# Kernel optimization log

Hardware: AMD Instinct MI355X
Metric: run time of the kernel (lower is better)

## Reference

```python
import jax, jax.numpy as jnp
import numpy as np

# ---- hash-grid constants (from tcnn Encoding config in __init__) ----
N_LEVELS = 16
F = 2                      # n_features_per_level
LOG2_T = 19
T = 1 << LOG2_T            # hashmap entries per level
BASE_RES = 16
PER_LEVEL_SCALE = 1.447269237440378
PRIMES = np.array([1, 2654435761, 805459861], dtype=np.uint32)
# corner offsets of the unit cube, shape [8, 3]
OFFS = np.stack(np.meshgrid([0, 1], [0, 1], [0, 1], indexing='ij'), -1).reshape(8, 3)


def hash_grid_encode(x01, table):
    """x01: [N,3] in [0,1]; table: [L, T, F]. Returns [N, L*F]."""
    offs = jnp.asarray(OFFS, dtype=jnp.int32)          # [8,3]
    primes = jnp.asarray(PRIMES)                       # [3] uint32
    feats = []
    for l in range(N_LEVELS):
        scale = BASE_RES * (PER_LEVEL_SCALE ** l) - 1.0   # tcnn grid scale
        res = int(np.ceil(scale)) + 1                      # grid resolution
        pos = x01 * scale + 0.5                            # [N,3]
        pos0 = jnp.floor(pos)
        w = pos - pos0                                     # trilinear fracs [N,3]
        pos0 = pos0.astype(jnp.int32)
        corners = jnp.clip(pos0[:, None, :] + offs[None], 0, res - 1)  # [N,8,3]
        if res ** 3 <= T:
            # dense (stride) indexing fits in the table
            idx = (corners[..., 0]
                   + res * corners[..., 1]
                   + res * res * corners[..., 2]).astype(jnp.int32)    # [N,8]
        else:
            # spatial hash with uint32 wraparound multiply + xor
            cu = corners.astype(jnp.uint32)
            idx = ((cu[..., 0] * primes[0])
                   ^ (cu[..., 1] * primes[1])
                   ^ (cu[..., 2] * primes[2])) & jnp.uint32(T - 1)
            idx = idx.astype(jnp.int32)
        # trilinear weights: prod over dims of (w if offset==1 else 1-w)
        wc = jnp.where(offs[None].astype(bool), w[:, None, :], 1.0 - w[:, None, :])
        wc = wc.prod(-1)                                   # [N,8]
        g = table[l][idx]                                  # gather -> [N,8,F]
        feats.append(jnp.einsum('nc,ncf->nf', wc, g))      # [N,F]
    return jnp.concatenate(feats, -1)                      # [N, L*F]


def mlp2(x, w1, w2):
    # 2-layer bias-free MLP with ReLU, matching MLP(num_layers=2, bias=False)
    return jnp.maximum(x @ w1, 0.0) @ w2


def setup_inputs() -> dict:
    key = jax.random.key(0)
    ks = jax.random.split(key, 6)
    N = 1048576
    points = jax.random.uniform(ks[0], (N, 3), jnp.float32, -1.0, 1.0)  # in bbox [-1,1]^3
    # tcnn hash-grid init: uniform(-1e-4, 1e-4)
    hash_table = jax.random.uniform(ks[1], (N_LEVELS, T, F), jnp.float32, -1e-4, 1e-4)
    enc_dim = N_LEVELS * F  # 32
    dw1 = jax.random.normal(ks[2], (enc_dim, 64), jnp.float32) * (1.0 / np.sqrt(enc_dim))
    dw2 = jax.random.normal(ks[3], (64, 1), jnp.float32) * (1.0 / 8.0)
    fw1 = jax.random.normal(ks[4], (enc_dim, 64), jnp.float32) * (1.0 / np.sqrt(enc_dim))
    fw2 = jax.random.normal(ks[5], (64, 3), jnp.float32) * (1.0 / 8.0)
    return {"points": points, "hash_table": hash_table,
            "dw1": dw1, "dw2": dw2, "fw1": fw1, "fw2": fw2}


def reference(points, hash_table, dw1, dw2, fw1, fw2):
    # contract_to_unisphere with bbox [[-1,-1,-1],[1,1,1]] -> [0,1]^3, clamped
    x01 = jnp.clip((points + 1.0) * 0.5, 0.0, 1.0)
    enc = hash_grid_encode(x01, hash_table)               # [N, 32]
    density = jax.nn.softplus(mlp2(enc, dw1, dw2))        # [N, 1]
    color = jax.nn.sigmoid(mlp2(enc, fw1, fw2))           # [N, 3]
    return color, density
```

## Files before the change

### kernel.cpp

```cpp
#include <hip/hip_runtime.h>
#include <hip/hip_bf16.h>
#include <cmath>

#define NLV 16
#define TBL_SIZE (1u << 19)

#define SORT_PPB 8192
#define SORT_THREADS 512
#define SORT_NKEYS 4096

#define KB15 32768
#define PPB2 4096
#define GS_THREADS 1024

struct LevelConsts {
    float scale[NLV];
    int   res[NLV];
    int   dense[NLV];
};

__device__ __forceinline__ unsigned int f32_to_bf16_rne(float f) {
    unsigned int u = __float_as_uint(f);
    return (u + 0x7FFFu + ((u >> 16) & 1u)) >> 16;
}
__device__ __forceinline__ unsigned int pack_bf16(float a, float b) {
    return f32_to_bf16_rne(a) | (f32_to_bf16_rne(b) << 16);
}
__device__ __forceinline__ short f32_to_bf16_s(float f) {
    return (short)f32_to_bf16_rne(f);
}
__device__ __forceinline__ float bf16lo_to_f32(unsigned int g) {
    return __uint_as_float(g << 16);
}
__device__ __forceinline__ float bf16hi_to_f32(unsigned int g) {
    return __uint_as_float(g & 0xFFFF0000u);
}

typedef __attribute__((ext_vector_type(8))) short bf16x8;
typedef __attribute__((ext_vector_type(4))) float f32x4;
typedef __attribute__((ext_vector_type(2))) unsigned int u32x2;
typedef __attribute__((ext_vector_type(4))) unsigned int u32x4;

__device__ __forceinline__ unsigned spread3(unsigned x) {
    x &= 0x3FFu;
    x = (x | (x << 16)) & 0x030000FFu;
    x = (x | (x << 8))  & 0x0300F00Fu;
    x = (x | (x << 4))  & 0x030C30C3u;
    x = (x | (x << 2))  & 0x09249249u;
    return x;
}
__device__ __forceinline__ unsigned key12(float px, float py, float pz) {
    float x = fminf(fmaxf((px + 1.0f) * 0.5f, 0.0f), 1.0f);
    float y = fminf(fmaxf((py + 1.0f) * 0.5f, 0.0f), 1.0f);
    float z = fminf(fmaxf((pz + 1.0f) * 0.5f, 0.0f), 1.0f);
    int ix = min((int)(x * 16.0f), 15);
    int iy = min((int)(y * 16.0f), 15);
    int iz = min((int)(z * 16.0f), 15);
    return spread3((unsigned)ix) | (spread3((unsigned)iy) << 1) | (spread3((unsigned)iz) << 2);
}
__device__ __forceinline__ unsigned key15(float px, float py, float pz) {
    float x = fminf(fmaxf((px + 1.0f) * 0.5f, 0.0f), 1.0f);
    float y = fminf(fmaxf((py + 1.0f) * 0.5f, 0.0f), 1.0f);
    float z = fminf(fmaxf((pz + 1.0f) * 0.5f, 0.0f), 1.0f);
    int ix = min((int)(x * 32.0f), 31);
    int iy = min((int)(y * 32.0f), 31);
    int iz = min((int)(z * 32.0f), 31);
    return spread3((unsigned)ix) | (spread3((unsigned)iy) << 1) | (spread3((unsigned)iz) << 2);
}

__global__ __launch_bounds__(GS_THREADS) void cvt_and_hist(
    const float* __restrict__ tablef32, unsigned int* __restrict__ tbl_out, int npairs,
    const float* __restrict__ pts, unsigned int* __restrict__ colpre32,
    int N, int histBlocks)
{
    __shared__ unsigned packed[KB15 / 2];
    if ((int)blockIdx.x < histBlocks) {
        const int blk = blockIdx.x, base = blk * PPB2, cnt = min(PPB2, N - base);
        const int tid = threadIdx.x;
        for (int i = tid; i < KB15 / 2; i += GS_THREADS) packed[i] = 0u;
        __syncthreads();
#pragma unroll
        for (int q = 0; q < PPB2 / GS_THREADS; q++) {
            int idx = q * GS_THREADS + tid;
            if (idx < cnt) {
                int p = base + idx;
                unsigned k = key15(pts[3 * p + 0], pts[3 * p + 1], pts[3 * p + 2]);
                atomicAdd(&packed[k >> 1], (k & 1u) ? 0x10000u : 1u);
            }
        }
        __syncthreads();
        for (int i = tid; i < KB15 / 2; i += GS_THREADS)
            colpre32[(size_t)blk * (KB15 / 2) + i] = packed[i];
    } else {
        int b = blockIdx.x - histBlocks;
        int n2 = npairs >> 1;
        int i = b * GS_THREADS + threadIdx.x;
        int stride = ((int)gridDim.x - histBlocks) * GS_THREADS;
        const f32x4* in4 = (const f32x4*)tablef32;
        u32x2* out2 = (u32x2*)tbl_out;
        for (; i < n2; i += stride) {
            f32x4 v = __builtin_nontemporal_load(&in4[i]);
            u32x2 o;
            o.x = pack_bf16(v.x, v.y);
            o.y = pack_bf16(v.z, v.w);
            __builtin_nontemporal_store(o, &out2[i]);
        }
    }
}

__global__ __launch_bounds__(GS_THREADS) void colscan(
    unsigned int* __restrict__ colpre32, unsigned int* __restrict__ tot, int nblk)
{
    int k2 = blockIdx.x * GS_THREADS + threadIdx.x;
    unsigned run0 = 0, run1 = 0;
    for (int b = 0; b < nblk; b++) {
        size_t off = (size_t)b * (KB15 / 2) + k2;
        unsigned v = colpre32[off];
        colpre32[off] = run0 | (run1 << 16);
        run0 += v & 0xFFFFu;
        run1 += v >> 16;
    }
    tot[2 * k2 + 0] = run0;
    tot[2 * k2 + 1] = run1;
}

__global__ __launch_bounds__(GS_THREADS) void scan_tot(unsigned int* __restrict__ tot) {
    __shared__ unsigned wsum[GS_THREADS / 64];
    const int t = threadIdx.x, lane = t & 63, wid = t >> 6;
    unsigned loc[KB15 / GS_THREADS];
    unsigned s = 0;
#pragma unroll
    for (int j = 0; j < KB15 / GS_THREADS; j++) { loc[j] = tot[t * (KB15 / GS_THREADS) + j]; s += loc[j]; }
    unsigned x = s;
#pragma unroll
    for (int d = 1; d < 64; d <<= 1) {
        unsigned y = __shfl_up(x, d, 64);
        if (lane >= d) x += y;
    }
    unsigned wex = x - s;
    if (lane == 63) wsum[wid] = x;
    __syncthreads();
    if (t == 0) {
        unsigned r = 0;
        for (int i = 0; i < GS_THREADS / 64; i++) { unsigned tt = wsum[i]; wsum[i] = r; r += tt; }
    }
    __syncthreads();
    unsigned run = wex + wsum[wid];
#pragma unroll
    for (int j = 0; j < KB15 / GS_THREADS; j++) { tot[t * (KB15 / GS_THREADS) + j] = run; run += loc[j]; }
}

__global__ __launch_bounds__(GS_THREADS) void global_scatter(
    const float* __restrict__ pts, const unsigned int* __restrict__ colpre32,
    const unsigned int* __restrict__ tot, f32x4* __restrict__ spts4, int N)
{
    __shared__ unsigned packed[KB15 / 2];
    const int blk = blockIdx.x, base = blk * PPB2, cnt = min(PPB2, N - base);
    const int tid = threadIdx.x;
    for (int i = tid; i < KB15 / 2; i += GS_THREADS) packed[i] = 0u;
    __syncthreads();
#pragma unroll
    for (int q = 0; q < PPB2 / GS_THREADS; q++) {
        int idx = q * GS_THREADS + tid;
        if (idx < cnt) {
            int p = base + idx;
            float px = pts[3 * p + 0];
            float py = pts[3 * p + 1];
            float pz = pts[3 * p + 2];
            unsigned k = key15(px, py, pz);
            unsigned old = atomicAdd(&packed[k >> 1], (k & 1u) ? 0x10000u : 1u);
            unsigned rank = (old >> ((k & 1u) * 16)) & 0xFFFFu;
            unsigned cb = colpre32[(size_t)blk * (KB15 / 2) + (k >> 1)];
            unsigned colbase = (k & 1u) ? (cb >> 16) : (cb & 0xFFFFu);
            unsigned pos = tot[k] + colbase + rank;
            f32x4 o;
            o.x = px; o.y = py; o.z = pz; o.w = __uint_as_float((unsigned)p);
            spts4[pos] = o;
        }
    }
}

__global__ __launch_bounds__(SORT_THREADS) void cvt_and_sort(
    const float* __restrict__ tablef32, unsigned int* __restrict__ tbl_out, int npairs,
    const float* __restrict__ pts, f32x4* __restrict__ spts4, int N, int sortBlocks)
{
    __shared__ unsigned hist[SORT_NKEYS];
    __shared__ unsigned wsum[SORT_THREADS / 64];

    if ((int)blockIdx.x < sortBlocks) {
        const int sb   = blockIdx.x;
        const int base = sb * SORT_PPB;
        const int cnt  = min(SORT_PPB, N - base);
        const int tid  = threadIdx.x;
        const int lane = tid & 63, wid = tid >> 6;

        for (int i = tid; i < SORT_NKEYS; i += SORT_THREADS) hist[i] = 0u;
        __syncthreads();

        unsigned short keys[16];
#pragma unroll
        for (int q = 0; q < 16; q++) {
            int idx = q * SORT_THREADS + tid;
            unsigned k = 0xFFFFu;
            if (idx < cnt) {
                int p = base + idx;
                k = key12(pts[3 * p + 0], pts[3 * p + 1], pts[3 * p + 2]);
                atomicAdd(&hist[k], 1u);
            }
            keys[q] = (unsigned short)k;
        }
        __syncthreads();

        unsigned loc[8], s = 0;
#pragma unroll
        for (int j = 0; j < 8; j++) { loc[j] = hist[tid * 8 + j]; s += loc[j]; }
        unsigned x = s;
#pragma unroll
        for (int d = 1; d < 64; d <<= 1) {
            unsigned y = __shfl_up(x, d, 64);
            if (lane >= d) x += y;
        }
        unsigned wex = x - s;
        if (lane == 63) wsum[wid] = x;
        __syncthreads();
        if (tid == 0) {
            unsigned r = 0;
            for (int i = 0; i < SORT_THREADS / 64; i++) { unsigned t2 = wsum[i]; wsum[i] = r; r += t2; }
        }
        __syncthreads();
        unsigned run = wex + wsum[wid];
#pragma unroll
        for (int j = 0; j < 8; j++) { hist[tid * 8 + j] = run; run += loc[j]; }
        __syncthreads();

#pragma unroll
        for (int q = 0; q < 16; q++) {
            int idx = q * SORT_THREADS + tid;
            if (idx < cnt) {
                int p = base + idx;
                float px = pts[3 * p + 0];
                float py = pts[3 * p + 1];
                float pz = pts[3 * p + 2];
                unsigned pos = atomicAdd(&hist[keys[q]], 1u);
                f32x4 o;
                o.x = px; o.y = py; o.z = pz; o.w = __uint_as_float((unsigned)p);
                spts4[base + pos] = o;
            }
        }
    } else {
        int b = blockIdx.x - sortBlocks;
        int n2 = npairs >> 1;
        int i = b * SORT_THREADS + threadIdx.x;
        int stride = ((int)gridDim.x - sortBlocks) * SORT_THREADS;
        const f32x4* in4 = (const f32x4*)tablef32;
        u32x2* out2 = (u32x2*)tbl_out;
        for (; i < n2; i += stride) {
            f32x4 v = __builtin_nontemporal_load(&in4[i]);
            u32x2 o;
            o.x = pack_bf16(v.x, v.y);
            o.y = pack_bf16(v.z, v.w);
            __builtin_nontemporal_store(o, &out2[i]);
        }
    }
}

__global__ __launch_bounds__(256) void cvt_table(const float* __restrict__ in,
                                                 unsigned int* __restrict__ out, int npairs) {
    int n2 = npairs >> 1;
    int i = blockIdx.x * 256 + threadIdx.x;
    int stride = gridDim.x * 256;
    const f32x4* in4 = (const f32x4*)in;
    u32x2* out2 = (u32x2*)out;
    for (; i < n2; i += stride) {
        f32x4 v = __builtin_nontemporal_load(&in4[i]);
        u32x2 o;
        o.x = pack_bf16(v.x, v.y);
        o.y = pack_bf16(v.z, v.w);
        __builtin_nontemporal_store(o, &out2[i]);
    }
}

#define ENC_P 4
template<int PSTRIDE>
__global__ __launch_bounds__(256) void encode_lvl(
    const float* __restrict__ points,
    const unsigned int* __restrict__ tbl,
    unsigned int* __restrict__ enc,
    int N, LevelConsts C)
{
    const int level = blockIdx.y;
    const float sc    = C.scale[level];
    const int   res   = C.res[level];
    const int   dense = C.dense[level];
    const unsigned int* __restrict__ t = tbl + (size_t)level * TBL_SIZE;
    unsigned int* __restrict__ eo = enc + (size_t)level * N;

    const int base = blockIdx.x * (256 * ENC_P) + threadIdx.x;

    int   pt[ENC_P];
    int   valid[ENC_P];
    float wx[ENC_P], wy[ENC_P], wz[ENC_P];
    unsigned int i0a[ENC_P][4], i1a[ENC_P][4];

#pragma unroll
    for (int q = 0; q < ENC_P; q++) {
        pt[q] = base + q * 256;
        valid[q] = pt[q] < N;
        int p = valid[q] ? pt[q] : 0;
        float px, py, pz;
        if (PSTRIDE == 4) {
            f32x4 v = *(const f32x4*)&points[(size_t)p * 4];
            px = v.x; py = v.y; pz = v.z;
        } else {
            px = points[p * 3 + 0];
            py = points[p * 3 + 1];
            pz = points[p * 3 + 2];
        }
        float x = fminf(fmaxf((px + 1.0f) * 0.5f, 0.0f), 1.0f);
        float y = fminf(fmaxf((py + 1.0f) * 0.5f, 0.0f), 1.0f);
        float z = fminf(fmaxf((pz + 1.0f) * 0.5f, 0.0f), 1.0f);

        float fx = x * sc + 0.5f;
        float fy = y * sc + 0.5f;
        float fz = z * sc + 0.5f;
        float f0x = floorf(fx), f0y = floorf(fy), f0z = floorf(fz);
        wx[q] = fx - f0x; wy[q] = fy - f0y; wz[q] = fz - f0z;
        int ix0 = min(max((int)f0x, 0), res - 1);
        int iy0 = min(max((int)f0y, 0), res - 1);
        int iz0 = min(max((int)f0z, 0), res - 1);
        int ix1 = min(ix0 + 1, res - 1);
        int iy1 = min(iy0 + 1, res - 1);
        int iz1 = min(iz0 + 1, res - 1);

#pragma unroll
        for (int m = 0; m < 4; m++) {
            unsigned int uy = (unsigned int)((m & 1) ? iy1 : iy0);
            unsigned int uz = (unsigned int)((m & 2) ? iz1 : iz0);
            unsigned int i0, i1;
            if (dense) {
                unsigned int b = (unsigned int)res * uy + (unsigned int)(res * res) * uz;
                i0 = (unsigned int)ix0 + b;
                i1 = (unsigned int)ix1 + b;
            } else {
                unsigned int H = uy * 2654435761u ^ uz * 805459861u;
                i0 = ((unsigned int)ix0 ^ H) & (TBL_SIZE - 1u);
                i1 = ((unsigned int)ix1 ^ H) & (TBL_SIZE - 1u);
            }
            i0a[q][m] = i0;
            i1a[q][m] = i1;
        }
    }

    u32x2 pr[ENC_P][4];
#pragma unroll
    for (int q = 0; q < ENC_P; q++)
#pragma unroll
        for (int m = 0; m < 4; m++)
            pr[q][m] = *(const u32x2*)(t + (i0a[q][m] & ~1u));

    unsigned int ex[ENC_P][4];
#pragma unroll
    for (int q = 0; q < ENC_P; q++)
#pragma unroll
        for (int m = 0; m < 4; m++) {
            unsigned int i0 = i0a[q][m], i1 = i1a[q][m];
            unsigned int e = 0u;
            if (i1 != (i0 ^ 1u)) e = t[i1];
            ex[q][m] = e;
        }

#pragma unroll
    for (int q = 0; q < ENC_P; q++) {
        float e0 = 0.0f, e1 = 0.0f;
        float wxq = wx[q];
#pragma unroll
        for (int m = 0; m < 4; m++) {
            unsigned int i0 = i0a[q][m], i1 = i1a[q][m];
            u32x2 P = pr[q][m];
            unsigned int v0   = (i0 & 1u) ? P.y : P.x;
            unsigned int vpar = (i0 & 1u) ? P.x : P.y;
            unsigned int v1   = (i1 == (i0 ^ 1u)) ? vpar : ex[q][m];
            float wyz = (((m & 1) ? wy[q] : 1.0f - wy[q])) *
                        (((m & 2) ? wz[q] : 1.0f - wz[q]));
            float w0 = wyz * (1.0f - wxq);
            float w1 = wyz * wxq;
            e0 = fmaf(w0, bf16lo_to_f32(v0), e0);
            e0 = fmaf(w1, bf16lo_to_f32(v1), e0);
            e1 = fmaf(w0, bf16hi_to_f32(v0), e1);
            e1 = fmaf(w1, bf16hi_to_f32(v1), e1);
        }
        if (valid[q]) __builtin_nontemporal_store(pack_bf16(e0, e1), &eo[pt[q]]);
    }
}

__global__ __launch_bounds__(256, 4) void mlp_kernel(
    const unsigned int* __restrict__ enc,
    const float* __restrict__ dw1, const float* __restrict__ dw2,
    const float* __restrict__ fw1, const float* __restrict__ fw2,
    const unsigned int* __restrict__ perm,
    float* __restrict__ out, int N, int ntiles)
{
    __shared__ unsigned int hsh[4][16][68];
    __shared__ float sOut[4][256];

    const int tid  = threadIdx.x;
    const int wave = tid >> 6;
    const int lane = tid & 63;
    const int l15 = lane & 15;
    const int quad = lane >> 4;

    bf16x8 B1[8];
#pragma unroll
    for (int nt = 0; nt < 8; nt++) {
        int col = nt * 16 + l15;
        const float* w = (col < 64) ? (dw1 + col) : (fw1 + (col - 64));
#pragma unroll
        for (int j = 0; j < 8; j++) {
            int k = quad * 8 + j;
            B1[nt][j] = f32_to_bf16_s(w[k * 64]);
        }
    }

    bf16x8 B2[4];
#pragma unroll
    for (int s = 0; s < 4; s++) {
#pragma unroll
        for (int j = 0; j < 8; j++) {
            int k_lds = s * 32 + quad * 8 + j;
            int hu = ((k_lds & 7) << 4) | (k_lds >> 3);
            float v = 0.0f;
            if (l15 == 0)      v = (hu < 64)  ? dw2[hu] : 0.0f;
            else if (l15 < 4)  v = (hu >= 64) ? fw2[(hu - 64) * 3 + (l15 - 1)] : 0.0f;
            B2[s][j] = f32_to_bf16_s(v);
        }
    }

    for (int tile = blockIdx.x; tile < ntiles; tile += gridDim.x) {
        const int wbase = tile * 256 + wave * 64;

        unsigned int au[4][4];
#pragma unroll
        for (int sub = 0; sub < 4; sub++) {
            int ptc = min(wbase + sub * 16 + l15, N - 1);
#pragma unroll
            for (int j = 0; j < 4; j++)
                au[sub][j] = enc[(size_t)(quad * 4 + j) * N + ptc];
        }

#pragma unroll
        for (int sub = 0; sub < 4; sub++) {
            union { unsigned int u[4]; bf16x8 v; } acvt;
#pragma unroll
            for (int j = 0; j < 4; j++) acvt.u[j] = au[sub][j];

            f32x4 acc1[8];
#pragma unroll
            for (int nt = 0; nt < 8; nt++) {
                acc1[nt] = (f32x4){0.0f, 0.0f, 0.0f, 0.0f};
                acc1[nt] = __builtin_amdgcn_mfma_f32_16x16x32_bf16(acvt.v, B1[nt], acc1[nt], 0, 0, 0);
            }

#pragma unroll
            for (int r = 0; r < 4; r++) {
                u32x4 pk;
#pragma unroll
                for (int d = 0; d < 4; d++) {
                    float h0 = fmaxf(acc1[2 * d + 0][r], 0.0f);
                    float h1 = fmaxf(acc1[2 * d + 1][r], 0.0f);
                    pk[d] = pack_bf16(h0, h1);
                }
                *(u32x4*)&hsh[wave][quad * 4 + r][l15 * 4] = pk;
            }

            f32x4 p0 = (f32x4){0,0,0,0}, p1 = (f32x4){0,0,0,0};
            f32x4 p2 = (f32x4){0,0,0,0}, p3 = (f32x4){0,0,0,0};
            {
                bf16x8 a0 = *(const bf16x8*)&hsh[wave][l15][0 * 16 + quad * 4];
                bf16x8 a1 = *(const bf16x8*)&hsh[wave][l15][1 * 16 + quad * 4];
                bf16x8 a2 = *(const bf16x8*)&hsh[wave][l15][2 * 16 + quad * 4];
                bf16x8 a3 = *(const bf16x8*)&hsh[wave][l15][3 * 16 + quad * 4];
                p0 = __builtin_amdgcn_mfma_f32_16x16x32_bf16(a0, B2[0], p0, 0, 0, 0);
                p1 = __builtin_amdgcn_mfma_f32_16x16x32_bf16(a1, B2[1], p1, 0, 0, 0);
                p2 = __builtin_amdgcn_mfma_f32_16x16x32_bf16(a2, B2[2], p2, 0, 0, 0);
                p3 = __builtin_amdgcn_mfma_f32_16x16x32_bf16(a3, B2[3], p3, 0, 0, 0);
            }
            f32x4 acc2;
#pragma unroll
            for (int r = 0; r < 4; r++) acc2[r] = (p0[r] + p1[r]) + (p2[r] + p3[r]);

            if (l15 < 4) {
#pragma unroll
                for (int r = 0; r < 4; r++)
                    sOut[wave][(sub * 16 + quad * 4 + r) * 4 + l15] = acc2[r];
            }
        }

        if (perm) {
            int p = wbase + lane;
            if (p < N) {
                unsigned int o = perm[(size_t)p * 4 + 3];
                f32x4 v = *(const f32x4*)&sOut[wave][lane * 4];
                float d = v[0];
                d = (d > 20.0f) ? d : log1pf(expf(d));
                out[(size_t)3 * N + o] = d;
                float r0 = 1.0f / (1.0f + expf(-v[1]));
                float g0 = 1.0f / (1.0f + expf(-v[2]));
                float b0 = 1.0f / (1.0f + expf(-v[3]));
                out[(size_t)o * 3 + 0] = r0;
                out[(size_t)o * 3 + 1] = g0;
                out[(size_t)o * 3 + 2] = b0;
            }
        } else {
            long long cmax = ((long long)N - wbase) * 3;
#pragma unroll
            for (int round = 0; round < 3; round++) {
                int f = round * 64 + lane;
                int lp = f / 3, c = f - lp * 3;
                float v = sOut[wave][lp * 4 + 1 + c];
                v = 1.0f / (1.0f + expf(-v));
                if (f < cmax) out[(size_t)wbase * 3 + f] = v;
            }
            {
                int p = wbase + lane;
                float v = sOut[wave][lane * 4];
                v = (v > 20.0f) ? v : log1pf(expf(v));
                if (p < N) out[(size_t)3 * N + p] = v;
            }
        }
    }
}

__global__ __launch_bounds__(256) void nerf_fused(
    const float* __restrict__ points,
    const float* __restrict__ table,
    const float* __restrict__ dw1, const float* __restrict__ dw2,
    const float* __restrict__ fw1, const float* __restrict__ fw2,
    float* __restrict__ out, int N, LevelConsts C)
{
    __shared__ float sD[64 * 32];
    __shared__ float sF[64 * 32];
    __shared__ float sDw2[64];
    __shared__ float sFw2[64 * 3];

    for (int idx = threadIdx.x; idx < 2048; idx += 256) {
        int i = idx >> 6;
        int j = idx & 63;
        sD[j * 32 + i] = dw1[idx];
        sF[j * 32 + i] = fw1[idx];
    }
    if (threadIdx.x < 64)  sDw2[threadIdx.x] = dw2[threadIdx.x];
    if (threadIdx.x < 192) sFw2[threadIdx.x] = fw2[threadIdx.x];
    __syncthreads();

    int gid = blockIdx.x * 256 + threadIdx.x;
    if (gid >= N) return;

    float px = points[gid * 3 + 0];
    float py = points[gid * 3 + 1];
    float pz = points[gid * 3 + 2];
    float x = fminf(fmaxf((px + 1.0f) * 0.5f, 0.0f), 1.0f);
    float y = fminf(fmaxf((py + 1.0f) * 0.5f, 0.0f), 1.0f);
    float z = fminf(fmaxf((pz + 1.0f) * 0.5f, 0.0f), 1.0f);

    float enc[32];

#pragma unroll
    for (int l = 0; l < NLV; l++) {
        const float sc = C.scale[l];
        const int   res = C.res[l];
        const int   dense = C.dense[l];
        const float* __restrict__ tbl = table + (size_t)l * TBL_SIZE * 2;

        float fx = x * sc + 0.5f;
        float fy = y * sc + 0.5f;
        float fz = z * sc + 0.5f;
        float f0x = floorf(fx), f0y = floorf(fy), f0z = floorf(fz);
        float wx = fx - f0x, wy = fy - f0y, wz = fz - f0z;
        int ix0 = min(max((int)f0x, 0), res - 1);
        int iy0 = min(max((int)f0y, 0), res - 1);
        int iz0 = min(max((int)f0z, 0), res - 1);
        int ix1 = min(ix0 + 1, res - 1);
        int iy1 = min(iy0 + 1, res - 1);
        int iz1 = min(iz0 + 1, res - 1);

        float e0 = 0.0f, e1 = 0.0f;
#pragma unroll
        for (int c = 0; c < 8; c++) {
            int cx = (c & 4) ? ix1 : ix0;
            int cy = (c & 2) ? iy1 : iy0;
            int cz = (c & 1) ? iz1 : iz0;
            float wgt = (((c & 4) ? wx : 1.0f - wx) *
                         ((c & 2) ? wy : 1.0f - wy)) *
                         ((c & 1) ? wz : 1.0f - wz);
            unsigned int idx;
            if (dense) {
                idx = (unsigned int)(cx + res * cy + res * res * cz);
            } else {
                idx = ((unsigned int)cx * 1u
                     ^ (unsigned int)cy * 2654435761u
                     ^ (unsigned int)cz * 805459861u) & (TBL_SIZE - 1u);
            }
            const float2 g = *(const float2*)(tbl + (size_t)idx * 2);
            e0 = fmaf(wgt, g.x, e0);
            e1 = fmaf(wgt, g.y, e1);
        }
        enc[2 * l + 0] = e0;
        enc[2 * l + 1] = e1;
    }

    float dacc = 0.0f, c0 = 0.0f, c1 = 0.0f, c2 = 0.0f;
    for (int j = 0; j < 64; j++) {
        float hd = 0.0f, hf = 0.0f;
        const float* __restrict__ colD = &sD[j * 32];
        const float* __restrict__ colF = &sF[j * 32];
#pragma unroll
        for (int i = 0; i < 32; i++) {
            hd = fmaf(enc[i], colD[i], hd);
            hf = fmaf(enc[i], colF[i], hf);
        }
        hd = fmaxf(hd, 0.0f);
        hf = fmaxf(hf, 0.0f);
        dacc = fmaf(hd, sDw2[j], dacc);
        c0 = fmaf(hf, sFw2[j * 3 + 0], c0);
        c1 = fmaf(hf, sFw2[j * 3 + 1], c1);
        c2 = fmaf(hf, sFw2[j * 3 + 2], c2);
    }

    float density = (dacc > 20.0f) ? dacc : log1pf(expf(dacc));
    out[gid * 3 + 0] = 1.0f / (1.0f + expf(-c0));
    out[gid * 3 + 1] = 1.0f / (1.0f + expf(-c1));
    out[gid * 3 + 2] = 1.0f / (1.0f + expf(-c2));
    out[(size_t)3 * N + gid] = density;
}

extern "C" void kernel_launch(void* const* d_in, const int* in_sizes, int n_in,
                              void* d_out, int out_size, void* d_ws, size_t ws_size,
                              hipStream_t stream) {
    const float* points = (const float*)d_in[0];
    const float* table  = (const float*)d_in[1];
    const float* dw1    = (const float*)d_in[2];
    const float* dw2    = (const float*)d_in[3];
    const float* fw1    = (const float*)d_in[4];
    const float* fw2    = (const float*)d_in[5];
    int N = in_sizes[0] / 3;

    LevelConsts C;
    for (int l = 0; l < NLV; l++) {
        double s = 16.0 * pow(1.447269237440378, (double)l) - 1.0;
        C.scale[l] = (float)s;
        int res = (int)ceil(s) + 1;
        C.res[l] = res;
        C.dense[l] = ((long long)res * res * res <= (long long)TBL_SIZE) ? 1 : 0;
    }

    auto align256 = [](size_t x) { return (x + 255) & ~(size_t)255; };
    const size_t tbl_bytes  = align256((size_t)NLV * TBL_SIZE * 4);
    const size_t enc_bytes  = align256((size_t)N * NLV * 4);
    const size_t spts_bytes = align256((size_t)N * 4 * 4);

    int nblk = (N + PPB2 - 1) / PPB2;
    const size_t colpre_bytes = align256((size_t)nblk * (KB15 / 2) * 4);
    const size_t tot_bytes    = align256((size_t)KB15 * 4);

    int ntiles = (N + 255) / 256;
    int chunks = (N + 256 * ENC_P - 1) / (256 * ENC_P);
    int npairs = NLV * TBL_SIZE;

    if (ws_size >= tbl_bytes + enc_bytes + spts_bytes &&
        enc_bytes >= colpre_bytes + tot_bytes) {
        char* wp = (char*)d_ws;
        unsigned int* tbl_bf16 = (unsigned int*)wp;            wp += tbl_bytes;
        unsigned int* enc_ws   = (unsigned int*)wp;            wp += enc_bytes;
        f32x4*        spts4    = (f32x4*)wp;                   wp += spts_bytes;
        unsigned int* colpre   = enc_ws;
        unsigned int* tot      = (unsigned int*)((char*)enc_ws + colpre_bytes);

        cvt_and_hist<<<nblk + 512, GS_THREADS, 0, stream>>>(
            table, tbl_bf16, npairs, points, colpre, N, nblk);
        colscan<<<KB15 / 2 / GS_THREADS, GS_THREADS, 0, stream>>>(colpre, tot, nblk);
        scan_tot<<<1, GS_THREADS, 0, stream>>>(tot);
        global_scatter<<<nblk, GS_THREADS, 0, stream>>>(points, colpre, tot, spts4, N);

        encode_lvl<4><<<dim3(chunks, NLV), 256, 0, stream>>>((const float*)spts4,
                                                             tbl_bf16, enc_ws, N, C);
        mlp_kernel<<<1792, 256, 0, stream>>>(enc_ws, dw1, dw2, fw1, fw2,
                                             (const unsigned int*)spts4,
                                             (float*)d_out, N, ntiles);
    } else if (ws_size >= tbl_bytes + enc_bytes + spts_bytes) {
        char* wp = (char*)d_ws;
        unsigned int* tbl_bf16 = (unsigned int*)wp;            wp += tbl_bytes;
        unsigned int* enc_ws   = (unsigned int*)wp;            wp += enc_bytes;
        f32x4*        spts4    = (f32x4*)wp;                   wp += spts_bytes;

        int sortBlocks = (N + SORT_PPB - 1) / SORT_PPB;
        cvt_and_sort<<<sortBlocks + 1024, SORT_THREADS, 0, stream>>>(
            table, tbl_bf16, npairs, points, spts4, N, sortBlocks);

        encode_lvl<4><<<dim3(chunks, NLV), 256, 0, stream>>>((const float*)spts4,
                                                             tbl_bf16, enc_ws, N, C);
        mlp_kernel<<<1792, 256, 0, stream>>>(enc_ws, dw1, dw2, fw1, fw2,
                                             (const unsigned int*)spts4,
                                             (float*)d_out, N, ntiles);
    } else if (ws_size >= tbl_bytes + enc_bytes) {
        unsigned int* tbl_bf16 = (unsigned int*)d_ws;
        unsigned int* enc_ws   = (unsigned int*)((char*)d_ws + tbl_bytes);

        cvt_table<<<1024, 256, 0, stream>>>(table, tbl_bf16, npairs);
        encode_lvl<3><<<dim3(chunks, NLV), 256, 0, stream>>>(points, tbl_bf16, enc_ws, N, C);
        mlp_kernel<<<1792, 256, 0, stream>>>(enc_ws, dw1, dw2, fw1, fw2, nullptr,
                                             (float*)d_out, N, ntiles);
    } else {
        int blocks = (N + 255) / 256;
        nerf_fused<<<blocks, 256, 0, stream>>>(points, table, dw1, dw2, fw1, fw2,
                                               (float*)d_out, N, C);
    }
}
```

Baseline: 542.2 us.

## Replace LDS-ranked scatter with global-atomic cursor scatter and widen histogram chunks

The histogram chunk size grows from 4096 to 16384 points, so there are fewer per-block column prefixes to scan. The colscan kernel now runs with many small blocks and an unrolled loop. The shared-memory ranked global_scatter is replaced by scatter_cursor, a grid-stride kernel that takes each point's output slot with atomicAdd directly on the scanned colpre cursors, which removes the per-block LDS clear and rank pass. The cost is contended global atomics and a nondeterministic order within each key bucket. mlp_kernel also stages dw1/fw1 through LDS for coalesced weight loading and caps its grid at 1024 blocks.

```diff
diff --git a/kernel.cpp b/kernel.cpp
--- a/kernel.cpp
+++ b/kernel.cpp
@@ -10,8 +10,10 @@
 #define SORT_NKEYS 4096
 
 #define KB15 32768
-#define PPB2 4096
+#define PPB2 16384
 #define GS_THREADS 1024
+#define CSCAN_THREADS 64
+#define SCAN_THREADS 1024
 
 struct LevelConsts {
     float scale[NLV];
@@ -108,12 +110,28 @@
     }
 }
 
-__global__ __launch_bounds__(GS_THREADS) void colscan(
+__global__ __launch_bounds__(CSCAN_THREADS) void colscan(
     unsigned int* __restrict__ colpre32, unsigned int* __restrict__ tot, int nblk)
 {
-    int k2 = blockIdx.x * GS_THREADS + threadIdx.x;
+    int k2 = blockIdx.x * CSCAN_THREADS + threadIdx.x;
     unsigned run0 = 0, run1 = 0;
-    for (int b = 0; b < nblk; b++) {
+    int b = 0;
+    for (; b + 4 <= nblk; b += 4) {
+        size_t o0 = (size_t)b * (KB15 / 2) + k2;
+        unsigned v0 = colpre32[o0];
+        unsigned v1 = colpre32[o0 + (size_t)(KB15 / 2)];
+        unsigned v2 = colpre32[o0 + (size_t)2 * (KB15 / 2)];
+        unsigned v3 = colpre32[o0 + (size_t)3 * (KB15 / 2)];
+        colpre32[o0] = run0 | (run1 << 16);
+        run0 += v0 & 0xFFFFu; run1 += v0 >> 16;
+        colpre32[o0 + (size_t)(KB15 / 2)] = run0 | (run1 << 16);
+        run0 += v1 & 0xFFFFu; run1 += v1 >> 16;
+        colpre32[o0 + (size_t)2 * (KB15 / 2)] = run0 | (run1 << 16);
+        run0 += v2 & 0xFFFFu; run1 += v2 >> 16;
+        colpre32[o0 + (size_t)3 * (KB15 / 2)] = run0 | (run1 << 16);
+        run0 += v3 & 0xFFFFu; run1 += v3 >> 16;
+    }
+    for (; b < nblk; b++) {
         size_t off = (size_t)b * (KB15 / 2) + k2;
         unsigned v = colpre32[off];
         colpre32[off] = run0 | (run1 << 16);
@@ -124,13 +142,13 @@
     tot[2 * k2 + 1] = run1;
 }
 
-__global__ __launch_bounds__(GS_THREADS) void scan_tot(unsigned int* __restrict__ tot) {
-    __shared__ unsigned wsum[GS_THREADS / 64];
+__global__ __launch_bounds__(SCAN_THREADS) void scan_tot(unsigned int* __restrict__ tot) {
+    __shared__ unsigned wsum[SCAN_THREADS / 64];
     const int t = threadIdx.x, lane = t & 63, wid = t >> 6;
-    unsigned loc[KB15 / GS_THREADS];
+    unsigned loc[KB15 / SCAN_THREADS];
     unsigned s = 0;
 #pragma unroll
-    for (int j = 0; j < KB15 / GS_THREADS; j++) { loc[j] = tot[t * (KB15 / GS_THREADS) + j]; s += loc[j]; }
+    for (int j = 0; j < KB15 / SCAN_THREADS; j++) { loc[j] = tot[t * (KB15 / SCAN_THREADS) + j]; s += loc[j]; }
     unsigned x = s;
 #pragma unroll
     for (int d = 1; d < 64; d <<= 1) {
@@ -142,41 +160,33 @@
     __syncthreads();
     if (t == 0) {
         unsigned r = 0;
-        for (int i = 0; i < GS_THREADS / 64; i++) { unsigned tt = wsum[i]; wsum[i] = r; r += tt; }
+        for (int i = 0; i < SCAN_THREADS / 64; i++) { unsigned tt = wsum[i]; wsum[i] = r; r += tt; }
     }
     __syncthreads();
     unsigned run = wex + wsum[wid];
 #pragma unroll
-    for (int j = 0; j < KB15 / GS_THREADS; j++) { tot[t * (KB15 / GS_THREADS) + j] = run; run += loc[j]; }
-}
-
-__global__ __launch_bounds__(GS_THREADS) void global_scatter(
-    const float* __restrict__ pts, const unsigned int* __restrict__ colpre32,
+    for (int j = 0; j < KB15 / SCAN_THREADS; j++) { tot[t * (KB15 / SCAN_THREADS) + j] = run; run += loc[j]; }
+}
+
+__global__ __launch_bounds__(256) void scatter_cursor(
+    const float* __restrict__ pts, unsigned int* __restrict__ colpre32,
     const unsigned int* __restrict__ tot, f32x4* __restrict__ spts4, int N)
 {
-    __shared__ unsigned packed[KB15 / 2];
-    const int blk = blockIdx.x, base = blk * PPB2, cnt = min(PPB2, N - base);
-    const int tid = threadIdx.x;
-    for (int i = tid; i < KB15 / 2; i += GS_THREADS) packed[i] = 0u;
-    __syncthreads();
-#pragma unroll
-    for (int q = 0; q < PPB2 / GS_THREADS; q++) {
-        int idx = q * GS_THREADS + tid;
-        if (idx < cnt) {
-            int p = base + idx;
-            float px = pts[3 * p + 0];
-            float py = pts[3 * p + 1];
-            float pz = pts[3 * p + 2];
-            unsigned k = key15(px, py, pz);
-            unsigned old = atomicAdd(&packed[k >> 1], (k & 1u) ? 0x10000u : 1u);
-            unsigned rank = (old >> ((k & 1u) * 16)) & 0xFFFFu;
-            unsigned cb = colpre32[(size_t)blk * (KB15 / 2) + (k >> 1)];
-            unsigned colbase = (k & 1u) ? (cb >> 16) : (cb & 0xFFFFu);
-            unsigned pos = tot[k] + colbase + rank;
-            f32x4 o;
-            o.x = px; o.y = py; o.z = pz; o.w = __uint_as_float((unsigned)p);
-            spts4[pos] = o;
-        }
+    int i = blockIdx.x * 256 + threadIdx.x;
+    int stride = gridDim.x * 256;
+    for (; i < N; i += stride) {
+        float px = pts[3 * i + 0];
+        float py = pts[3 * i + 1];
+        float pz = pts[3 * i + 2];
+        unsigned k = key15(px, py, pz);
+        unsigned w = (unsigned)i / PPB2;
+        unsigned old = atomicAdd(&colpre32[(size_t)w * (KB15 / 2) + (k >> 1)],
+                                 (k & 1u) ? 0x10000u : 1u);
+        unsigned cr = (k & 1u) ? (old >> 16) : (old & 0xFFFFu);
+        unsigned pos = tot[k] + cr;
+        f32x4 o;
+        o.x = px; o.y = py; o.z = pz; o.w = __uint_as_float((unsigned)i);
+        spts4[pos] = o;
     }
 }
 
@@ -409,17 +419,28 @@
     const int l15 = lane & 15;
     const int quad = lane >> 4;
 
+    float* sW = (float*)hsh;
     bf16x8 B1[8];
-#pragma unroll
-    for (int nt = 0; nt < 8; nt++) {
+    for (int i = tid; i < 2048; i += 256) sW[i] = dw1[i];
+    __syncthreads();
+#pragma unroll
+    for (int nt = 0; nt < 4; nt++) {
         int col = nt * 16 + l15;
-        const float* w = (col < 64) ? (dw1 + col) : (fw1 + (col - 64));
-#pragma unroll
-        for (int j = 0; j < 8; j++) {
-            int k = quad * 8 + j;
-            B1[nt][j] = f32_to_bf16_s(w[k * 64]);
-        }
-    }
+#pragma unroll
+        for (int j = 0; j < 8; j++)
+            B1[nt][j] = f32_to_bf16_s(sW[(quad * 8 + j) * 64 + col]);
+    }
+    __syncthreads();
+    for (int i = tid; i < 2048; i += 256) sW[i] = fw1[i];
+    __syncthreads();
+#pragma unroll
+    for (int nt = 4; nt < 8; nt++) {
+        int col = nt * 16 + l15 - 64;
+#pragma unroll
+        for (int j = 0; j < 8; j++)
+            B1[nt][j] = f32_to_bf16_s(sW[(quad * 8 + j) * 64 + col]);
+    }
+    __syncthreads();
 
     bf16x8 B2[4];
 #pragma unroll
@@ -677,13 +698,13 @@
 
         cvt_and_hist<<<nblk + 512, GS_THREADS, 0, stream>>>(
             table, tbl_bf16, npairs, points, colpre, N, nblk);
-        colscan<<<KB15 / 2 / GS_THREADS, GS_THREADS, 0, stream>>>(colpre, tot, nblk);
-        scan_tot<<<1, GS_THREADS, 0, stream>>>(tot);
-        global_scatter<<<nblk, GS_THREADS, 0, stream>>>(points, colpre, tot, spts4, N);
+        colscan<<<(KB15 / 2) / CSCAN_THREADS, CSCAN_THREADS, 0, stream>>>(colpre, tot, nblk);
+        scan_tot<<<1, SCAN_THREADS, 0, stream>>>(tot);
+        scatter_cursor<<<1024, 256, 0, stream>>>(points, colpre, tot, spts4, N);
 
         encode_lvl<4><<<dim3(chunks, NLV), 256, 0, stream>>>((const float*)spts4,
                                                              tbl_bf16, enc_ws, N, C);
-        mlp_kernel<<<1792, 256, 0, stream>>>(enc_ws, dw1, dw2, fw1, fw2,
+        mlp_kernel<<<min(ntiles, 1024), 256, 0, stream>>>(enc_ws, dw1, dw2, fw1, fw2,
                                              (const unsigned int*)spts4,
                                              (float*)d_out, N, ntiles);
     } else if (ws_size >= tbl_bytes + enc_bytes + spts_bytes) {
@@ -698,7 +719,7 @@
 
         encode_lvl<4><<<dim3(chunks, NLV), 256, 0, stream>>>((const float*)spts4,
                                                              tbl_bf16, enc_ws, N, C);
-        mlp_kernel<<<1792, 256, 0, stream>>>(enc_ws, dw1, dw2, fw1, fw2,
+        mlp_kernel<<<min(ntiles, 1024), 256, 0, stream>>>(enc_ws, dw1, dw2, fw1, fw2,
                                              (const unsigned int*)spts4,
                                              (float*)d_out, N, ntiles);
     } else if (ws_size >= tbl_bytes + enc_bytes) {
@@ -707,7 +728,7 @@
 
         cvt_table<<<1024, 256, 0, stream>>>(table, tbl_bf16, npairs);
         encode_lvl<3><<<dim3(chunks, NLV), 256, 0, stream>>>(points, tbl_bf16, enc_ws, N, C);
-        mlp_kernel<<<1792, 256, 0, stream>>>(enc_ws, dw1, dw2, fw1, fw2, nullptr,
+        mlp_kernel<<<min(ntiles, 1024), 256, 0, stream>>>(enc_ws, dw1, dw2, fw1, fw2, nullptr,
                                              (float*)d_out, N, ntiles);
     } else {
         int blocks = (N + 255) / 256;
```

After: 508.0 us. -6.3%, faster.
